# Performance work log

Measured on AMD Instinct MI355X. Metric: run time of the kernel, lower is better.

The kernel has to match this reference:

```python
import jax, jax.numpy as jnp
import numpy as np

N = 4096          # nodes (= Mamba sequence length)
E_EDGES = 65536   # edges
D = 512           # dim_h (= d_inner, expand=1)
NEXP = 4          # num_experts (cfg.model.num_experts)
DSTATE = 16
DCONV = 4
DTRANK = 32       # ceil(D/16)
EPS = 1e-5


def _silu(x):
    return x * jax.nn.sigmoid(x)


def _bn(h, g, b):
    # BatchNorm1d over node axis (batch statistics)
    mu = h.mean(0)
    var = h.var(0)
    return (h - mu) * jax.lax.rsqrt(var + EPS) * g + b


def _mamba(u, in_w, conv_w, conv_b, x_w, dt_w, dt_b, A_log, Dp, out_w):
    # u: [L, D] single-sequence Mamba(d_model=D, d_state=16, d_conv=4, expand=1)
    L = u.shape[0]
    xz = u @ in_w                      # [L, 2D]
    xc, z = xz[:, :D], xz[:, D:]
    xp = jnp.pad(xc, ((DCONV - 1, 0), (0, 0)))
    xconv = conv_b
    for k in range(DCONV):             # depthwise causal conv, tiny fixed loop
        xconv = xconv + conv_w[:, k] * xp[k:k + L]
    xs = _silu(xconv)                  # [L, D]
    dbc = xs @ x_w                     # [L, DTRANK + 2*DSTATE]
    dt = jax.nn.softplus(dbc[:, :DTRANK] @ dt_w + dt_b)          # [L, D]
    Bm = dbc[:, DTRANK:DTRANK + DSTATE]                          # [L, S]
    Cm = dbc[:, DTRANK + DSTATE:]                                # [L, S]
    A = -jnp.exp(A_log)                                          # [D, S]
    dA = jnp.exp(dt[:, :, None] * A[None])                       # [L, D, S]
    dBu = dt[:, :, None] * Bm[:, None, :] * xs[:, :, None]       # [L, D, S]

    def step(hprev, inp):
        dA_t, dBu_t, C_t = inp
        hn = dA_t * hprev + dBu_t
        return hn, (hn * C_t[None, :]).sum(-1)

    _, ys = jax.lax.scan(step, jnp.zeros((D, DSTATE), u.dtype), (dA, dBu, Cm))
    y = ys + Dp * xs
    return (y * _silu(z)) @ out_w      # [L, D]


def setup_inputs() -> dict:
    key = jax.random.key(0)
    ks = jax.random.split(key, 24)
    s = 1.0 / np.sqrt(D)
    inp = {}
    inp['x'] = jax.random.normal(ks[0], (N, D), jnp.float32)
    inp['edge_index'] = jax.random.randint(ks[1], (2, E_EDGES), 0, N)
    inp['edge_attr'] = jax.random.normal(ks[2], (E_EDGES, D), jnp.float32)
    # GINE nn: Linear(D,D) -> ReLU -> Linear(D,D)
    inp['gin_w1'] = jax.random.normal(ks[3], (D, D)) * s
    inp['gin_b1'] = jnp.zeros((D,))
    inp['gin_w2'] = jax.random.normal(ks[4], (D, D)) * s
    inp['gin_b2'] = jnp.zeros((D,))
    # BatchNorms
    inp['bn1l_g'] = jnp.ones((D,)); inp['bn1l_b'] = jnp.zeros((D,))
    inp['bn1a_g'] = jnp.ones((D,)); inp['bn1a_b'] = jnp.zeros((D,))
    inp['bn2_g'] = jnp.ones((D,)); inp['bn2_b'] = jnp.zeros((D,))
    # gating MLP [D, D//2, NEXP]
    inp['gate_w1'] = jax.random.normal(ks[5], (D, D // 2)) * s
    inp['gate_b1'] = jnp.zeros((D // 2,))
    inp['gate_w2'] = jax.random.normal(ks[6], (D // 2, NEXP)) * (1.0 / np.sqrt(D // 2))
    inp['gate_b2'] = jnp.zeros((NEXP,))
    # stacked per-expert Mamba params
    inp['in_w'] = jax.random.normal(ks[7], (NEXP, D, 2 * D)) * s
    inp['conv_w'] = jax.random.normal(ks[8], (NEXP, D, DCONV)) * 0.5
    inp['conv_b'] = jnp.zeros((NEXP, D))
    inp['x_w'] = jax.random.normal(ks[9], (NEXP, D, DTRANK + 2 * DSTATE)) * s
    inp['dt_w'] = jax.random.normal(ks[10], (NEXP, DTRANK, D)) * (1.0 / np.sqrt(DTRANK))
    inp['dt_b'] = jax.random.normal(ks[11], (NEXP, D)) * 0.1 - 4.0
    A0 = jnp.log(jnp.arange(1, DSTATE + 1, dtype=jnp.float32))
    inp['A_log'] = jnp.broadcast_to(A0, (NEXP, D, DSTATE)).copy()
    inp['Dp'] = jnp.ones((NEXP, D))
    inp['out_w'] = jax.random.normal(ks[12], (NEXP, D, D)) * s
    # FFN
    inp['ff_w1'] = jax.random.normal(ks[13], (D, 2 * D)) * s
    inp['ff_b1'] = jnp.zeros((2 * D,))
    inp['ff_w2'] = jax.random.normal(ks[14], (2 * D, D)) * (1.0 / np.sqrt(2 * D))
    inp['ff_b2'] = jnp.zeros((D,))
    return inp


def reference(x, edge_index, edge_attr,
              gin_w1, gin_b1, gin_w2, gin_b2,
              bn1l_g, bn1l_b, bn1a_g, bn1a_b, bn2_g, bn2_b,
              gate_w1, gate_b1, gate_w2, gate_b2,
              in_w, conv_w, conv_b, x_w, dt_w, dt_b, A_log, Dp, out_w,
              ff_w1, ff_b1, ff_w2, ff_b2):
    h_in = x
    src, dst = edge_index[0], edge_index[1]
    # local GINEConv: nn(x + sum_j relu(x_j + e_ji))
    msg = jax.nn.relu(x[src] + edge_attr)                      # [E, D]
    aggr = jax.ops.segment_sum(msg, dst, num_segments=N)       # [N, D]
    h_local = jax.nn.relu((x + aggr) @ gin_w1 + gin_b1) @ gin_w2 + gin_b2
    h_local = _bn(h_in + h_local, bn1l_g, bn1l_b)
    # gated mixture of Mamba experts
    gate = jax.nn.softmax(jax.nn.relu(x @ gate_w1 + gate_b1) @ gate_w2 + gate_b2, axis=-1)  # [N, NEXP]
    ys = jax.vmap(_mamba, in_axes=(None, 0, 0, 0, 0, 0, 0, 0, 0, 0))(
        x, in_w, conv_w, conv_b, x_w, dt_w, dt_b, A_log, Dp, out_w)  # [NEXP, N, D]
    h_attn = jnp.einsum('ne,end->nd', gate, ys)
    h_attn = _bn(h_in + h_attn, bn1a_g, bn1a_b)
    # fuse + FFN
    h = h_local + h_attn
    ff = jax.nn.relu(h @ ff_w1 + ff_b1) @ ff_w2 + ff_b2
    return _bn(h + ff, bn2_g, bn2_b)
```

## Files before the change

kernel.cpp:

```cpp
#include <hip/hip_runtime.h>
#include <hip/hip_bf16.h>
#include <math.h>

#define N_NODES 4096
#define E_EDGE 65536
#define D 512
#define NEXP 4
#define DSTATE 16
#define DCONV 4
#define DTRANK 32
#define EPS 1e-5f
#define LCHUNK 32
#define NCHUNK (N_NODES / LCHUNK)

typedef __hip_bfloat16 bf16;
typedef short bf16x8 __attribute__((ext_vector_type(8)));
typedef float f32x4 __attribute__((ext_vector_type(4)));
typedef unsigned short u16x4 __attribute__((ext_vector_type(4)));

__device__ __forceinline__ float siluf(float x) { return x / (1.f + __expf(-x)); }
__device__ __forceinline__ float softplusf(float x) {
  return (x > 20.f) ? x : log1pf(__expf(x));
}
__device__ __forceinline__ unsigned short f2bf(float v) {
  bf16 b = __float2bfloat16(v);
  return *reinterpret_cast<unsigned short*>(&b);
}

__device__ __forceinline__ void gload16(const void* g, void* l) {
  __builtin_amdgcn_global_load_lds(
      (const __attribute__((address_space(1))) void*)g,
      (__attribute__((address_space(3))) void*)l, 16, 0, 0);
}

template <int FN, int EPI, bool STATS>
__global__ __launch_bounds__(256, 2) void mm_k(
    const bf16* __restrict__ A, int lda, long sA,
    const bf16* __restrict__ Bt, int ldb, long sB,
    const float* __restrict__ bias,
    float* __restrict__ Cf, bf16* __restrict__ Cb, int ldc, long sC, int K,
    const float* __restrict__ part, float* __restrict__ sacc) {
  constexpr int BN = FN * 32;
  __shared__ __align__(16) bf16 As[2][128 * 32];
  __shared__ __align__(16) bf16 Bs[2][BN * 32];
  const int z = blockIdx.z;
  A += (size_t)z * sA;
  Bt += (size_t)z * sB;
  const int tid = threadIdx.x;
  const int w = tid >> 6, l = tid & 63;
  const int wr = w >> 1, wc = w & 1;
  const int bm = blockIdx.y * 128, bn = blockIdx.x * BN;

  f32x4 acc[4][FN];
#pragma unroll
  for (int i = 0; i < 4; ++i)
#pragma unroll
    for (int j = 0; j < FN; ++j) acc[i][j] = 0.f;

  const int srow = l >> 2, schunk = l & 3;
  const bf16* gA = A + (size_t)(bm + w * 16 + srow) * lda + schunk * 8;
  const bf16* gB = Bt + (size_t)(bn + w * 16 + srow) * ldb + schunk * 8;

  const int ar = wr * 64 + (l & 15);
  const int br = wc * FN * 16 + (l & 15);
  const int kb = l >> 4;

  auto stage = [&](int b, int k0) {
    gload16(gA + k0, As[b] + w * 512);
    gload16(gA + k0 + (size_t)64 * lda, As[b] + 64 * 32 + w * 512);
    gload16(gB + k0, Bs[b] + w * 512);
    if (FN == 4) gload16(gB + k0 + (size_t)64 * ldb, Bs[b] + 64 * 32 + w * 512);
  };

  stage(0, 0);
  __syncthreads();
  int cur = 0;
  for (int k0 = 0; k0 < K; k0 += 32) {
    if (k0 + 32 < K) stage(cur ^ 1, k0 + 32);
    const bf16x8* Ap = (const bf16x8*)As[cur];
    const bf16x8* Bp = (const bf16x8*)Bs[cur];
    bf16x8 af[4], bfr[FN];
#pragma unroll
    for (int i = 0; i < 4; ++i) af[i] = Ap[(ar + i * 16) * 4 + kb];
#pragma unroll
    for (int j = 0; j < FN; ++j) bfr[j] = Bp[(br + j * 16) * 4 + kb];
#pragma unroll
    for (int i = 0; i < 4; ++i)
#pragma unroll
      for (int j = 0; j < FN; ++j)
        acc[i][j] = __builtin_amdgcn_mfma_f32_16x16x32_bf16(bfr[j], af[i], acc[i][j], 0, 0, 0);
    __syncthreads();
    cur ^= 1;
  }

  if (Cf) Cf += (size_t)z * sC;
  if (Cb) Cb += (size_t)z * sC;
  const int r0 = bm + wr * 64 + (l & 15);
  const int cb0 = bn + wc * FN * 16 + ((l >> 4) << 2);
  f32x4 ssum[FN], ssq[FN];
  if (STATS) {
#pragma unroll
    for (int j = 0; j < FN; ++j) { ssum[j] = 0.f; ssq[j] = 0.f; }
  }
#pragma unroll
  for (int i = 0; i < 4; ++i) {
    const int row = r0 + i * 16;
#pragma unroll
    for (int j = 0; j < FN; ++j) {
      const int col = cb0 + j * 16;
      f32x4 v = acc[i][j];
      if (bias) v += *(const f32x4*)&bias[col];
      if (EPI == 1) {
#pragma unroll
        for (int r = 0; r < 4; ++r) v[r] = fmaxf(v[r], 0.f);
      }
      if (Cf) *(f32x4*)&Cf[(size_t)row * ldc + col] = v;
      if (Cb) {
        u16x4 u;
#pragma unroll
        for (int r = 0; r < 4; ++r) u[r] = f2bf(v[r]);
        *(u16x4*)&Cb[(size_t)row * ldc + col] = u;
      }
      if (STATS) {
        f32x4 p = *(const f32x4*)&part[(size_t)row * ldc + col];
        f32x4 t = v + p;
        ssum[j] += t;
        ssq[j] += t * t;
      }
    }
  }
  if (STATS) {
#pragma unroll
    for (int m = 1; m < 16; m <<= 1) {
#pragma unroll
      for (int j = 0; j < FN; ++j)
#pragma unroll
        for (int r = 0; r < 4; ++r) {
          ssum[j][r] += __shfl_xor(ssum[j][r], m);
          ssq[j][r] += __shfl_xor(ssq[j][r], m);
        }
    }
    if ((l & 15) == 0) {
#pragma unroll
      for (int j = 0; j < FN; ++j)
#pragma unroll
        for (int r = 0; r < 4; ++r) {
          atomicAdd(&sacc[cb0 + j * 16 + r], ssum[j][r]);
          atomicAdd(&sacc[512 + cb0 + j * 16 + r], ssq[j][r]);
        }
    }
  }
}

struct WtArgs {
  const float* in[8];
  bf16* out[8];
  int K[8], N[8], ldo[8];
  long sin[8], sout[8];
  int cum[8];
};
__global__ __launch_bounds__(256) void wtrans_all_k(WtArgs a) {
  __shared__ float t[32][33];
  int b = blockIdx.x;
  int i = 0;
  while (b >= a.cum[i]) ++i;
  int local = b - (i ? a.cum[i - 1] : 0);
  const int ntx = a.N[i] / 32;
  const int nty = a.K[i] / 32;
  const int perz = ntx * nty;
  const int z = local / perz;
  const int rem = local - z * perz;
  const int bx = rem % ntx, by = rem / ntx;
  const float* in = a.in[i] + (size_t)z * a.sin[i];
  bf16* out = a.out[i] + (size_t)z * a.sout[i];
  const int N = a.N[i], ldo = a.ldo[i];
  const int n0 = bx * 32, k0 = by * 32;
  const int tx = threadIdx.x & 31, ty = threadIdx.x >> 5;
  for (int r = ty; r < 32; r += 8) t[r][tx] = in[(size_t)(k0 + r) * N + n0 + tx];
  __syncthreads();
  for (int r = ty; r < 32; r += 8)
    out[(size_t)(n0 + r) * ldo + k0 + tx] = __float2bfloat16(t[tx][r]);
}

__global__ void hist_k(const int* __restrict__ ei, int* __restrict__ deg) {
  int e = blockIdx.x * 256 + threadIdx.x;
  if (e < E_EDGE) atomicAdd(&deg[ei[E_EDGE + e]], 1);
}

__global__ __launch_bounds__(1024) void prefix_k(const int* __restrict__ deg,
                                                 int* __restrict__ rowstart) {
  __shared__ int s[1024];
  int t = threadIdx.x;
  int base = t * 4;
  int d0 = deg[base], d1 = deg[base + 1], d2 = deg[base + 2], d3 = deg[base + 3];
  int sum = d0 + d1 + d2 + d3;
  s[t] = sum;
  __syncthreads();
  for (int off = 1; off < 1024; off <<= 1) {
    int v = (t >= off) ? s[t - off] : 0;
    __syncthreads();
    s[t] += v;
    __syncthreads();
  }
  int excl = s[t] - sum;
  rowstart[base] = excl;
  rowstart[base + 1] = excl + d0;
  rowstart[base + 2] = excl + d0 + d1;
  rowstart[base + 3] = excl + d0 + d1 + d2;
}

__global__ void scatter_k(const int* __restrict__ ei, const int* __restrict__ rowstart,
                          int* __restrict__ cnt, int* __restrict__ eid) {
  int e = blockIdx.x * 256 + threadIdx.x;
  if (e < E_EDGE) {
    int dst = ei[E_EDGE + e];
    int slot = rowstart[dst] + atomicAdd(&cnt[dst], 1);
    eid[slot] = e;
  }
}

__global__ __launch_bounds__(256) void aggr_gather_k(
    const float* __restrict__ x, const int* __restrict__ ei, const float* __restrict__ ea,
    const int* __restrict__ rowstart, const int* __restrict__ deg,
    const int* __restrict__ eid, bf16* __restrict__ hpre, bf16* __restrict__ xbf) {
  int n = blockIdx.x;
  int tid = threadIdx.x;
  int beg = rowstart[n];
  int end = beg + deg[n];
  float a0 = 0.f, a1 = 0.f;
  int i = beg;
  for (; i + 1 < end; i += 2) {
    int e0 = eid[i], e1 = eid[i + 1];
    int s0 = ei[e0], s1 = ei[e1];
    const float* x0 = x + (size_t)s0 * D;
    const float* e0p = ea + (size_t)e0 * D;
    const float* x1 = x + (size_t)s1 * D;
    const float* e1p = ea + (size_t)e1 * D;
    a0 += fmaxf(x0[tid] + e0p[tid], 0.f) + fmaxf(x1[tid] + e1p[tid], 0.f);
    a1 += fmaxf(x0[tid + 256] + e0p[tid + 256], 0.f) +
          fmaxf(x1[tid + 256] + e1p[tid + 256], 0.f);
  }
  if (i < end) {
    int e0 = eid[i];
    int s0 = ei[e0];
    const float* x0 = x + (size_t)s0 * D;
    const float* e0p = ea + (size_t)e0 * D;
    a0 += fmaxf(x0[tid] + e0p[tid], 0.f);
    a1 += fmaxf(x0[tid + 256] + e0p[tid + 256], 0.f);
  }
  float xv0 = x[(size_t)n * D + tid];
  float xv1 = x[(size_t)n * D + tid + 256];
  hpre[(size_t)n * D + tid] = __float2bfloat16(xv0 + a0);
  hpre[(size_t)n * D + tid + 256] = __float2bfloat16(xv1 + a1);
  xbf[(size_t)n * D + tid] = __float2bfloat16(xv0);
  xbf[(size_t)n * D + tid + 256] = __float2bfloat16(xv1);
}

__global__ __launch_bounds__(256) void gate2_k(const float* __restrict__ g1,
                                               const float* __restrict__ w2,
                                               const float* __restrict__ b2,
                                               float* __restrict__ gate) {
  int row = blockIdx.x * 4 + (threadIdx.x >> 6);
  int lane = threadIdx.x & 63;
  float a0 = 0.f, a1 = 0.f, a2 = 0.f, a3 = 0.f;
  for (int k = lane; k < 256; k += 64) {
    float v = g1[(size_t)row * 256 + k];
    a0 = fmaf(v, w2[k * 4 + 0], a0);
    a1 = fmaf(v, w2[k * 4 + 1], a1);
    a2 = fmaf(v, w2[k * 4 + 2], a2);
    a3 = fmaf(v, w2[k * 4 + 3], a3);
  }
#pragma unroll
  for (int off = 32; off; off >>= 1) {
    a0 += __shfl_down(a0, off);
    a1 += __shfl_down(a1, off);
    a2 += __shfl_down(a2, off);
    a3 += __shfl_down(a3, off);
  }
  if (lane == 0) {
    float l0 = a0 + b2[0], l1 = a1 + b2[1], l2 = a2 + b2[2], l3 = a3 + b2[3];
    float m = fmaxf(fmaxf(l0, l1), fmaxf(l2, l3));
    float e0 = __expf(l0 - m), e1 = __expf(l1 - m), e2 = __expf(l2 - m), e3 = __expf(l3 - m);
    float s = 1.f / (e0 + e1 + e2 + e3);
    gate[row * 4 + 0] = e0 * s;
    gate[row * 4 + 1] = e1 * s;
    gate[row * 4 + 2] = e2 * s;
    gate[row * 4 + 3] = e3 * s;
  }
}

__global__ void conv_silu_k(const bf16* __restrict__ xz, const float* __restrict__ cw,
                            const float* __restrict__ cb, bf16* __restrict__ xs, int e0) {
  const int z = blockIdx.y;
  xz += (size_t)z * N_NODES * 2 * D;
  xs += (size_t)z * N_NODES * D;
  cw += (size_t)(e0 + z) * D * DCONV;
  cb += (size_t)(e0 + z) * D;
  int idx = blockIdx.x * blockDim.x + threadIdx.x;
  if (idx >= N_NODES * D) return;
  int t = idx >> 9;
  int d = idx & (D - 1);
  float acc = cb[d];
#pragma unroll
  for (int k = 0; k < DCONV; ++k) {
    int tt = t + k - (DCONV - 1);
    if (tt >= 0)
      acc = fmaf(cw[d * DCONV + k], __bfloat162float(xz[(size_t)tt * (2 * D) + d]), acc);
  }
  xs[idx] = __float2bfloat16(siluf(acc));
}

__global__ void dt_k(const float* __restrict__ dbc, const float* __restrict__ dtw,
                     const float* __restrict__ dtbias, bf16* __restrict__ dt, int e0) {
  const int z = blockIdx.y;
  dbc += (size_t)z * N_NODES * 64;
  dt += (size_t)z * N_NODES * D;
  dtw += (size_t)(e0 + z) * DTRANK * D;
  dtbias += (size_t)(e0 + z) * D;
  int idx = blockIdx.x * blockDim.x + threadIdx.x;
  int t = idx >> 9, d = idx & (D - 1);
  float acc = dtbias[d];
#pragma unroll
  for (int k = 0; k < DTRANK; ++k) acc = fmaf(dbc[t * 64 + k], dtw[k * D + d], acc);
  dt[idx] = __float2bfloat16(softplusf(acc));
}

__device__ __forceinline__ void bn_params(const float* acc, int d, float& mu, float& rsig) {
  mu = acc[d] * (1.f / N_NODES);
  float var = acc[512 + d] * (1.f / N_NODES) - mu * mu;
  rsig = rsqrtf(var + EPS);
}

__global__ void norm_k(const float* __restrict__ p, const float* __restrict__ q,
                       const float* __restrict__ acc, const float* __restrict__ g,
                       const float* __restrict__ b, float* __restrict__ o) {
  int idx = blockIdx.x * blockDim.x + threadIdx.x;
  if (idx >= N_NODES * D) return;
  int d = idx & (D - 1);
  float mu, rsig;
  bn_params(acc, d, mu, rsig);
  o[idx] = (p[idx] + q[idx] - mu) * rsig * g[d] + b[d];
}

__global__ void bnadd2_k(const float* __restrict__ x, const float* __restrict__ hloc,
                         const float* __restrict__ hattn, const float* __restrict__ acc1,
                         const float* __restrict__ acc2, const float* __restrict__ g1,
                         const float* __restrict__ b1, const float* __restrict__ g2,
                         const float* __restrict__ b2, float* __restrict__ of,
                         bf16* __restrict__ ob) {
  int idx = blockIdx.x * blockDim.x + threadIdx.x;
  if (idx >= N_NODES * D) return;
  int d = idx & (D - 1);
  float mu1, rs1, mu2, rs2;
  bn_params(acc1, d, mu1, rs1);
  bn_params(acc2, d, mu2, rs2);
  float xv = x[idx];
  float v = (xv + hloc[idx] - mu1) * rs1 * g1[d] + b1[d] +
            (xv + hattn[idx] - mu2) * rs2 * g2[d] + b2[d];
  of[idx] = v;
  ob[idx] = __float2bfloat16(v);
}

__global__ __launch_bounds__(512) void scanA_k(const bf16* __restrict__ dt,
                                               const bf16* __restrict__ xs,
                                               const float* __restrict__ dbc,
                                               const float* __restrict__ Alog,
                                               float* __restrict__ Q,
                                               float* __restrict__ dtsum, int e0) {
  const int z = blockIdx.y;
  dt += (size_t)z * N_NODES * D;
  xs += (size_t)z * N_NODES * D;
  dbc += (size_t)z * N_NODES * 64;
  Alog += (size_t)(e0 + z) * D * DSTATE;
  Q += (size_t)z * NCHUNK * D * DSTATE;
  dtsum += (size_t)z * NCHUNK * D;
  int c = blockIdx.x;
  int d = threadIdx.x;
  float As[DSTATE], h[DSTATE];
#pragma unroll
  for (int s = 0; s < DSTATE; ++s) {
    As[s] = -__expf(Alog[d * DSTATE + s]);
    h[s] = 0.f;
  }
  float dts = 0.f;
  int t0 = c * LCHUNK;
  for (int t = t0; t < t0 + LCHUNK; ++t) {
    float dtv = __bfloat162float(dt[(size_t)t * D + d]);
    float xv = __bfloat162float(xs[(size_t)t * D + d]);
    float bx = dtv * xv;
    dts += dtv;
#pragma unroll
    for (int s = 0; s < DSTATE; ++s) {
      float Bv = dbc[(size_t)t * 64 + DTRANK + s];
      h[s] = fmaf(__expf(dtv * As[s]), h[s], bx * Bv);
    }
  }
  size_t base = ((size_t)c * D + d) * DSTATE;
#pragma unroll
  for (int s = 0; s < DSTATE; ++s) Q[base + s] = h[s];
  dtsum[c * D + d] = dts;
}

__global__ __launch_bounds__(256) void scanB_k(const float* __restrict__ Q,
                                               const float* __restrict__ dtsum,
                                               const float* __restrict__ Alog,
                                               float* __restrict__ Hin, int e0) {
  const int z = blockIdx.y;
  Q += (size_t)z * NCHUNK * D * DSTATE;
  dtsum += (size_t)z * NCHUNK * D;
  Alog += (size_t)(e0 + z) * D * DSTATE;
  Hin += (size_t)z * NCHUNK * D * DSTATE;
  int idx = blockIdx.x * blockDim.x + threadIdx.x;
  int d = idx >> 4;
  float As = -__expf(Alog[idx]);
  float h = 0.f;
  for (int c = 0; c < NCHUNK; ++c) {
    size_t base = (size_t)c * D * DSTATE + idx;
    Hin[base] = h;
    h = fmaf(__expf(As * dtsum[c * D + d]), h, Q[base]);
  }
}

__global__ __launch_bounds__(512) void scanC_k(const bf16* __restrict__ dt,
                                               const bf16* __restrict__ xs,
                                               const float* __restrict__ dbc,
                                               const float* __restrict__ Alog,
                                               const float* __restrict__ Hin,
                                               const bf16* __restrict__ xz,
                                               const float* __restrict__ Dp,
                                               const float* __restrict__ gate,
                                               bf16* __restrict__ u, int e0) {
  const int z = blockIdx.y;
  dt += (size_t)z * N_NODES * D;
  xs += (size_t)z * N_NODES * D;
  dbc += (size_t)z * N_NODES * 64;
  Alog += (size_t)(e0 + z) * D * DSTATE;
  Hin += (size_t)z * NCHUNK * D * DSTATE;
  xz += (size_t)z * N_NODES * 2 * D;
  Dp += (size_t)(e0 + z) * D;
  u += (size_t)(e0 + z) * 512;
  const int ge = e0 + z;
  int c = blockIdx.x;
  int d = threadIdx.x;
  float As[DSTATE], h[DSTATE];
  size_t base = ((size_t)c * D + d) * DSTATE;
#pragma unroll
  for (int s = 0; s < DSTATE; ++s) {
    As[s] = -__expf(Alog[d * DSTATE + s]);
    h[s] = Hin[base + s];
  }
  float Dv = Dp[d];
  int t0 = c * LCHUNK;
  for (int t = t0; t < t0 + LCHUNK; ++t) {
    float dtv = __bfloat162float(dt[(size_t)t * D + d]);
    float xv = __bfloat162float(xs[(size_t)t * D + d]);
    float bx = dtv * xv;
    float y = 0.f;
#pragma unroll
    for (int s = 0; s < DSTATE; ++s) {
      float Bv = dbc[(size_t)t * 64 + DTRANK + s];
      float Cv = dbc[(size_t)t * 64 + DTRANK + DSTATE + s];
      h[s] = fmaf(__expf(dtv * As[s]), h[s], bx * Bv);
      y = fmaf(h[s], Cv, y);
    }
    float zv = __bfloat162float(xz[(size_t)t * (2 * D) + D + d]);
    float gv = gate[t * NEXP + ge];
    u[(size_t)t * 2048 + d] = __float2bfloat16(gv * (y + Dv * xv) * siluf(zv));
  }
}

extern "C" void kernel_launch(void* const* d_in, const int* in_sizes, int n_in,
                              void* d_out, int out_size, void* d_ws, size_t ws_size,
                              hipStream_t stream) {
  const float* x = (const float*)d_in[0];
  const int* ei = (const int*)d_in[1];
  const float* ea = (const float*)d_in[2];
  const float* gin_w1 = (const float*)d_in[3];
  const float* gin_b1 = (const float*)d_in[4];
  const float* gin_w2 = (const float*)d_in[5];
  const float* gin_b2 = (const float*)d_in[6];
  const float* bn1l_g = (const float*)d_in[7];
  const float* bn1l_b = (const float*)d_in[8];
  const float* bn1a_g = (const float*)d_in[9];
  const float* bn1a_b = (const float*)d_in[10];
  const float* bn2_g = (const float*)d_in[11];
  const float* bn2_b = (const float*)d_in[12];
  const float* gate_w1 = (const float*)d_in[13];
  const float* gate_b1 = (const float*)d_in[14];
  const float* gate_w2 = (const float*)d_in[15];
  const float* gate_b2 = (const float*)d_in[16];
  const float* in_w = (const float*)d_in[17];
  const float* conv_w = (const float*)d_in[18];
  const float* conv_b = (const float*)d_in[19];
  const float* x_w = (const float*)d_in[20];
  const float* dt_w = (const float*)d_in[21];
  const float* dt_b = (const float*)d_in[22];
  const float* A_log = (const float*)d_in[23];
  const float* Dp = (const float*)d_in[24];
  const float* out_w = (const float*)d_in[25];
  const float* ff_w1 = (const float*)d_in[26];
  const float* ff_b1 = (const float*)d_in[27];
  const float* ff_w2 = (const float*)d_in[28];
  const float* ff_b2 = (const float*)d_in[29];
  float* out = (float*)d_out;

  const size_t ND = (size_t)N_NODES * D;
  const size_t NDb = ND / 2;

  const size_t fixed_f = 3 * ND + (size_t)N_NODES * 256 + 16384 + 2490624 + ND + 2048 +
                         81920 + 2 * ND + 4096;
  const size_t per_f = 2 * ND + NDb + (size_t)N_NODES * 64 + NDb +
                       2 * (size_t)NCHUNK * D * DSTATE + (size_t)NCHUNK * D;
  const int EB = (ws_size >= (fixed_f + 4 * per_f + 65536) * sizeof(float)) ? 4 : 1;

  float* ws = (float*)d_ws;
  size_t off = 0;
  auto alloc = [&](size_t n) {
    float* p = ws + off;
    off += (n + 63) & ~(size_t)63;
    return p;
  };
  float* ffo = alloc(ND);
  float* pbuf = alloc(ND);
  float* hlocal = alloc(ND);
  float* g1 = alloc((size_t)N_NODES * 256);
  float* gate = alloc((size_t)N_NODES * NEXP);
  bf16* gw1t = (bf16*)alloc(131072);
  bf16* gw2t = (bf16*)alloc(131072);
  bf16* gatew1t = (bf16*)alloc(65536);
  bf16* inwt = (bf16*)alloc(1048576);
  bf16* xwt = (bf16*)alloc(65536);
  bf16* outwt_cat = (bf16*)alloc(524288);
  bf16* ffw1t = (bf16*)alloc(262144);
  bf16* ffw2t = (bf16*)alloc(262144);
  int* deg = (int*)alloc(N_NODES);
  int* cnt = (int*)alloc(N_NODES);
  float* accs = alloc(3072);
  int* eid = (int*)alloc(E_EDGE);
  int* rowstart = (int*)alloc(N_NODES);
  float* xbf_f = alloc(NDb);
  float* xz_f = alloc((size_t)EB * ND);
  float* xs_f = alloc((size_t)EB * NDb);
  float* dbc = alloc((size_t)EB * N_NODES * 64);
  float* dtb_f = alloc((size_t)EB * NDb);
  float* Qb = alloc((size_t)EB * NCHUNK * D * DSTATE);
  float* Hin = alloc((size_t)EB * NCHUNK * D * DSTATE);
  float* dtsum = alloc((size_t)EB * NCHUNK * D);
  float* ucat_f = alloc(4 * NDb);
  float* hattn_raw = alloc(ND);
  float* acc1 = accs, *acc2 = accs + 1024, *acc3 = accs + 2048;

  bf16* x_bf = (bf16*)xbf_f;
  bf16* hpre_bf = (bf16*)pbuf;
  bf16* t1_bf = (bf16*)(pbuf + NDb);
  bf16* xz_bf = (bf16*)xz_f;
  bf16* xs_bf = (bf16*)xs_f;
  bf16* dt_bf = (bf16*)dtb_f;
  bf16* ucat = (bf16*)ucat_f;
  float* hcomb = xz_f;
  bf16* hcomb_bf = (bf16*)(ucat_f);
  bf16* ffh_bf = (bf16*)pbuf;

  const int nelem = N_NODES * D;
  const int ew = (nelem + 255) / 256;

  hipMemsetAsync(deg, 0, (N_NODES + N_NODES + 3072) * sizeof(float), stream);

  WtArgs wa;
  const float* wsrc[8] = {gin_w1, gin_w2, gate_w1, in_w, x_w, out_w, ff_w1, ff_w2};
  bf16* wdst[8] = {gw1t, gw2t, gatew1t, inwt, xwt, outwt_cat, ffw1t, ffw2t};
  int wK[8] = {512, 512, 512, 512, 512, 512, 512, 1024};
  int wN[8] = {512, 512, 256, 1024, 64, 512, 1024, 512};
  int wldo[8] = {512, 512, 512, 512, 512, 2048, 512, 1024};
  long wsin[8] = {0, 0, 0, (long)512 * 1024, (long)512 * 64, (long)512 * 512, 0, 0};
  long wsout[8] = {0, 0, 0, (long)512 * 1024, (long)64 * 512, 512, 0, 0};
  int wz[8] = {1, 1, 1, 4, 4, 4, 1, 1};
  int cum = 0;
  for (int i = 0; i < 8; ++i) {
    wa.in[i] = wsrc[i];
    wa.out[i] = wdst[i];
    wa.K[i] = wK[i];
    wa.N[i] = wN[i];
    wa.ldo[i] = wldo[i];
    wa.sin[i] = wsin[i];
    wa.sout[i] = wsout[i];
    cum += (wN[i] / 32) * (wK[i] / 32) * wz[i];
    wa.cum[i] = cum;
  }
  wtrans_all_k<<<cum, 256, 0, stream>>>(wa);

  hist_k<<<E_EDGE / 256, 256, 0, stream>>>(ei, deg);
  prefix_k<<<1, 1024, 0, stream>>>(deg, rowstart);
  scatter_k<<<E_EDGE / 256, 256, 0, stream>>>(ei, rowstart, cnt, eid);
  aggr_gather_k<<<N_NODES, 256, 0, stream>>>(x, ei, ea, rowstart, deg, eid, hpre_bf, x_bf);
  mm_k<2, 1, false><<<dim3(8, 32, 1), 256, 0, stream>>>(
      hpre_bf, 512, 0, gw1t, 512, 0, gin_b1, nullptr, t1_bf, 512, 0, 512, nullptr,
      nullptr);
  mm_k<2, 0, true><<<dim3(8, 32, 1), 256, 0, stream>>>(
      t1_bf, 512, 0, gw2t, 512, 0, gin_b2, hlocal, nullptr, 512, 0, 512, x, acc1);

  mm_k<2, 1, false><<<dim3(4, 32, 1), 256, 0, stream>>>(
      x_bf, 512, 0, gatew1t, 512, 0, gate_b1, g1, nullptr, 256, 0, 512, nullptr, nullptr);
  gate2_k<<<N_NODES / 4, 256, 0, stream>>>(g1, gate_w2, gate_b2, gate);

  for (int e0 = 0; e0 < NEXP; e0 += EB) {
    mm_k<4, 0, false><<<dim3(8, 32, EB), 256, 0, stream>>>(
        x_bf, 512, 0, inwt + (size_t)e0 * 512 * 1024, 512, (long)512 * 1024, nullptr,
        nullptr, xz_bf, 1024, (long)N_NODES * 1024, 512, nullptr, nullptr);
    conv_silu_k<<<dim3(ew, EB), 256, 0, stream>>>(xz_bf, conv_w, conv_b, xs_bf, e0);
    mm_k<2, 0, false><<<dim3(1, 32, EB), 256, 0, stream>>>(
        xs_bf, 512, (long)ND, xwt + (size_t)e0 * 64 * 512, 512, (long)64 * 512, nullptr,
        dbc, nullptr, 64, (long)N_NODES * 64, 512, nullptr, nullptr);
    dt_k<<<dim3(ew, EB), 256, 0, stream>>>(dbc, dt_w, dt_b, dt_bf, e0);
    scanA_k<<<dim3(NCHUNK, EB), 512, 0, stream>>>(dt_bf, xs_bf, dbc, A_log, Qb, dtsum, e0);
    scanB_k<<<dim3((D * DSTATE) / 256, EB), 256, 0, stream>>>(Qb, dtsum, A_log, Hin, e0);
    scanC_k<<<dim3(NCHUNK, EB), 512, 0, stream>>>(dt_bf, xs_bf, dbc, A_log, Hin, xz_bf, Dp,
                                                  gate, ucat, e0);
  }
  mm_k<2, 0, true><<<dim3(8, 32, 1), 256, 0, stream>>>(
      ucat, 2048, 0, outwt_cat, 2048, 0, nullptr, hattn_raw, nullptr, 512, 0, 2048, x,
      acc2);

  bnadd2_k<<<ew, 256, 0, stream>>>(x, hlocal, hattn_raw, acc1, acc2, bn1l_g, bn1l_b,
                                   bn1a_g, bn1a_b, hcomb, hcomb_bf);
  mm_k<4, 1, false><<<dim3(8, 32, 1), 256, 0, stream>>>(
      hcomb_bf, 512, 0, ffw1t, 512, 0, ff_b1, nullptr, ffh_bf, 1024, 0, 512, nullptr,
      nullptr);
  mm_k<2, 0, true><<<dim3(8, 32, 1), 256, 0, stream>>>(
      ffh_bf, 1024, 0, ffw2t, 1024, 0, ff_b2, ffo, nullptr, 512, 0, 1024, hcomb, acc3);
  norm_k<<<ew, 256, 0, stream>>>(hcomb, ffo, acc3, bn2_g, bn2_b, out);
}
```

Measured before the change: 464.6 us.

## Fuse CSR build into one kernel, vectorise conv/dt, raise mm occupancy

Replaces the histogram, prefix and scatter kernels and the memset with a single-block csr_build_k. It counts degrees and assigns slots with LDS atomics and also zeroes the BN accumulators, which removes several launches and global atomics. conv_silu_k and dt_k now handle four channels per thread with vector loads and stores, and mm_k with FN=2 asks for three blocks per CU in its launch bounds. The single-block CSR build serialises 65536 edges onto one CU, and the higher occupancy target may force register spills.

```diff
diff --git a/kernel.cpp b/kernel.cpp
--- a/kernel.cpp
+++ b/kernel.cpp
@@ -26,6 +26,11 @@
   bf16 b = __float2bfloat16(v);
   return *reinterpret_cast<unsigned short*>(&b);
 }
+__device__ __forceinline__ float bfu2f(unsigned short u) {
+  bf16 b;
+  *reinterpret_cast<unsigned short*>(&b) = u;
+  return __bfloat162float(b);
+}
 
 __device__ __forceinline__ void gload16(const void* g, void* l) {
   __builtin_amdgcn_global_load_lds(
@@ -34,7 +39,7 @@
 }
 
 template <int FN, int EPI, bool STATS>
-__global__ __launch_bounds__(256, 2) void mm_k(
+__global__ __launch_bounds__(256, FN == 2 ? 3 : 2) void mm_k(
     const bf16* __restrict__ A, int lda, long sA,
     const bf16* __restrict__ Bt, int ldb, long sB,
     const float* __restrict__ bias,
@@ -182,18 +187,23 @@
     out[(size_t)(n0 + r) * ldo + k0 + tx] = __float2bfloat16(t[tx][r]);
 }
 
-__global__ void hist_k(const int* __restrict__ ei, int* __restrict__ deg) {
-  int e = blockIdx.x * 256 + threadIdx.x;
-  if (e < E_EDGE) atomicAdd(&deg[ei[E_EDGE + e]], 1);
-}
-
-__global__ __launch_bounds__(1024) void prefix_k(const int* __restrict__ deg,
-                                                 int* __restrict__ rowstart) {
+__global__ __launch_bounds__(1024) void csr_build_k(const int* __restrict__ ei,
+                                                    int* __restrict__ deg,
+                                                    int* __restrict__ rowstart,
+                                                    int* __restrict__ eid,
+                                                    float* __restrict__ accs) {
+  __shared__ int degL[N_NODES];
   __shared__ int s[1024];
-  int t = threadIdx.x;
-  int base = t * 4;
-  int d0 = deg[base], d1 = deg[base + 1], d2 = deg[base + 2], d3 = deg[base + 3];
-  int sum = d0 + d1 + d2 + d3;
+  __shared__ int nextL[N_NODES];
+  const int t = threadIdx.x;
+  for (int i = t; i < 3072; i += 1024) accs[i] = 0.f;
+  for (int i = t; i < N_NODES; i += 1024) degL[i] = 0;
+  __syncthreads();
+  for (int e = t; e < E_EDGE; e += 1024) atomicAdd(&degL[ei[E_EDGE + e]], 1);
+  __syncthreads();
+  const int base = t * 4;
+  const int d0 = degL[base], d1 = degL[base + 1], d2 = degL[base + 2], d3 = degL[base + 3];
+  const int sum = d0 + d1 + d2 + d3;
   s[t] = sum;
   __syncthreads();
   for (int off = 1; off < 1024; off <<= 1) {
@@ -202,19 +212,23 @@
     s[t] += v;
     __syncthreads();
   }
-  int excl = s[t] - sum;
+  const int excl = s[t] - sum;
+  nextL[base] = excl;
+  nextL[base + 1] = excl + d0;
+  nextL[base + 2] = excl + d0 + d1;
+  nextL[base + 3] = excl + d0 + d1 + d2;
   rowstart[base] = excl;
   rowstart[base + 1] = excl + d0;
   rowstart[base + 2] = excl + d0 + d1;
   rowstart[base + 3] = excl + d0 + d1 + d2;
-}
-
-__global__ void scatter_k(const int* __restrict__ ei, const int* __restrict__ rowstart,
-                          int* __restrict__ cnt, int* __restrict__ eid) {
-  int e = blockIdx.x * 256 + threadIdx.x;
-  if (e < E_EDGE) {
+  deg[base] = d0;
+  deg[base + 1] = d1;
+  deg[base + 2] = d2;
+  deg[base + 3] = d3;
+  __syncthreads();
+  for (int e = t; e < E_EDGE; e += 1024) {
     int dst = ei[E_EDGE + e];
-    int slot = rowstart[dst] + atomicAdd(&cnt[dst], 1);
+    int slot = atomicAdd(&nextL[dst], 1);
     eid[slot] = e;
   }
 }
@@ -297,17 +311,25 @@
   cw += (size_t)(e0 + z) * D * DCONV;
   cb += (size_t)(e0 + z) * D;
   int idx = blockIdx.x * blockDim.x + threadIdx.x;
-  if (idx >= N_NODES * D) return;
-  int t = idx >> 9;
-  int d = idx & (D - 1);
-  float acc = cb[d];
+  if (idx >= N_NODES * (D / 4)) return;
+  int t = idx >> 7;
+  int d4 = (idx & 127) << 2;
+  float a[4];
+#pragma unroll
+  for (int j = 0; j < 4; ++j) a[j] = cb[d4 + j];
 #pragma unroll
   for (int k = 0; k < DCONV; ++k) {
     int tt = t + k - (DCONV - 1);
-    if (tt >= 0)
-      acc = fmaf(cw[d * DCONV + k], __bfloat162float(xz[(size_t)tt * (2 * D) + d]), acc);
-  }
-  xs[idx] = __float2bfloat16(siluf(acc));
+    if (tt >= 0) {
+      u16x4 v = *(const u16x4*)&xz[(size_t)tt * (2 * D) + d4];
+#pragma unroll
+      for (int j = 0; j < 4; ++j) a[j] = fmaf(cw[(d4 + j) * DCONV + k], bfu2f(v[j]), a[j]);
+    }
+  }
+  u16x4 o;
+#pragma unroll
+  for (int j = 0; j < 4; ++j) o[j] = f2bf(siluf(a[j]));
+  *(u16x4*)&xs[(size_t)t * D + d4] = o;
 }
 
 __global__ void dt_k(const float* __restrict__ dbc, const float* __restrict__ dtw,
@@ -318,11 +340,20 @@
   dtw += (size_t)(e0 + z) * DTRANK * D;
   dtbias += (size_t)(e0 + z) * D;
   int idx = blockIdx.x * blockDim.x + threadIdx.x;
-  int t = idx >> 9, d = idx & (D - 1);
-  float acc = dtbias[d];
-#pragma unroll
-  for (int k = 0; k < DTRANK; ++k) acc = fmaf(dbc[t * 64 + k], dtw[k * D + d], acc);
-  dt[idx] = __float2bfloat16(softplusf(acc));
+  if (idx >= N_NODES * (D / 4)) return;
+  int t = idx >> 7;
+  int d4 = (idx & 127) << 2;
+  f32x4 a = *(const f32x4*)&dtbias[d4];
+#pragma unroll
+  for (int k = 0; k < DTRANK; ++k) {
+    float b = dbc[t * 64 + k];
+    f32x4 wv = *(const f32x4*)&dtw[k * D + d4];
+    a += b * wv;
+  }
+  u16x4 o;
+#pragma unroll
+  for (int j = 0; j < 4; ++j) o[j] = f2bf(softplusf(a[j]));
+  *(u16x4*)&dt[(size_t)t * D + d4] = o;
 }
 
 __device__ __forceinline__ void bn_params(const float* acc, int d, float& mu, float& rsig) {
@@ -534,7 +565,6 @@
   bf16* ffw1t = (bf16*)alloc(262144);
   bf16* ffw2t = (bf16*)alloc(262144);
   int* deg = (int*)alloc(N_NODES);
-  int* cnt = (int*)alloc(N_NODES);
   float* accs = alloc(3072);
   int* eid = (int*)alloc(E_EDGE);
   int* rowstart = (int*)alloc(N_NODES);
@@ -563,8 +593,7 @@
 
   const int nelem = N_NODES * D;
   const int ew = (nelem + 255) / 256;
-
-  hipMemsetAsync(deg, 0, (N_NODES + N_NODES + 3072) * sizeof(float), stream);
+  const int ew4 = (nelem / 4 + 255) / 256;
 
   WtArgs wa;
   const float* wsrc[8] = {gin_w1, gin_w2, gate_w1, in_w, x_w, out_w, ff_w1, ff_w2};
@@ -589,9 +618,7 @@
   }
   wtrans_all_k<<<cum, 256, 0, stream>>>(wa);
 
-  hist_k<<<E_EDGE / 256, 256, 0, stream>>>(ei, deg);
-  prefix_k<<<1, 1024, 0, stream>>>(deg, rowstart);
-  scatter_k<<<E_EDGE / 256, 256, 0, stream>>>(ei, rowstart, cnt, eid);
+  csr_build_k<<<1, 1024, 0, stream>>>(ei, deg, rowstart, eid, accs);
   aggr_gather_k<<<N_NODES, 256, 0, stream>>>(x, ei, ea, rowstart, deg, eid, hpre_bf, x_bf);
   mm_k<2, 1, false><<<dim3(8, 32, 1), 256, 0, stream>>>(
       hpre_bf, 512, 0, gw1t, 512, 0, gin_b1, nullptr, t1_bf, 512, 0, 512, nullptr,
@@ -607,11 +634,11 @@
     mm_k<4, 0, false><<<dim3(8, 32, EB), 256, 0, stream>>>(
         x_bf, 512, 0, inwt + (size_t)e0 * 512 * 1024, 512, (long)512 * 1024, nullptr,
         nullptr, xz_bf, 1024, (long)N_NODES * 1024, 512, nullptr, nullptr);
-    conv_silu_k<<<dim3(ew, EB), 256, 0, stream>>>(xz_bf, conv_w, conv_b, xs_bf, e0);
+    conv_silu_k<<<dim3(ew4, EB), 256, 0, stream>>>(xz_bf, conv_w, conv_b, xs_bf, e0);
     mm_k<2, 0, false><<<dim3(1, 32, EB), 256, 0, stream>>>(
         xs_bf, 512, (long)ND, xwt + (size_t)e0 * 64 * 512, 512, (long)64 * 512, nullptr,
         dbc, nullptr, 64, (long)N_NODES * 64, 512, nullptr, nullptr);
-    dt_k<<<dim3(ew, EB), 256, 0, stream>>>(dbc, dt_w, dt_b, dt_bf, e0);
+    dt_k<<<dim3(ew4, EB), 256, 0, stream>>>(dbc, dt_w, dt_b, dt_bf, e0);
     scanA_k<<<dim3(NCHUNK, EB), 512, 0, stream>>>(dt_bf, xs_bf, dbc, A_log, Qb, dtsum, e0);
     scanB_k<<<dim3((D * DSTATE) / 256, EB), 256, 0, stream>>>(Qb, dtsum, A_log, Hin, e0);
     scanC_k<<<dim3(NCHUNK, EB), 512, 0, stream>>>(dt_bf, xs_bf, dbc, A_log, Hin, xz_bf, Dp,
```

Result: slower. 517.9 us (+11.5%).
